# Kernel tuning notes

Hardware: AMD Instinct MI355X
Metric: run time of the kernel (lower is better)

## Reference

```python
import jax, jax.numpy as jnp
import numpy as np

NUM_BIRDS = 512
NUM_COLORS = 512
HIDDEN = 128
NUM_LAYERS = 3


def setup_inputs() -> dict:
    key = jax.random.key(0)
    ks = jax.random.split(key, 12)
    s = 0.05
    H = HIDDEN
    L = NUM_LAYERS
    inp = {
        "probs": jax.random.uniform(ks[0], (NUM_BIRDS, NUM_COLORS), dtype=jnp.float32),
        "node_proj_w": jax.random.normal(ks[1], (NUM_COLORS, H), dtype=jnp.float32) * s,
        "node_proj_b": jnp.zeros((H,), dtype=jnp.float32),
        "edge_w1": jax.random.normal(ks[2], (L, 2 * H, H), dtype=jnp.float32) * s,
        "edge_b1": jnp.zeros((L, H), dtype=jnp.float32),
        "edge_w2": jax.random.normal(ks[3], (L, H, H), dtype=jnp.float32) * s,
        "edge_b2": jnp.zeros((L, H), dtype=jnp.float32),
        "node_w1": jax.random.normal(ks[4], (L, 2 * H, H), dtype=jnp.float32) * s,
        "node_b1": jnp.zeros((L, H), dtype=jnp.float32),
        "node_w2": jax.random.normal(ks[5], (L, H, H), dtype=jnp.float32) * s,
        "node_b2": jnp.zeros((L, H), dtype=jnp.float32),
        "color_proj_w": jax.random.normal(ks[6], (H, NUM_COLORS), dtype=jnp.float32) * s,
        "color_proj_b": jnp.zeros((NUM_COLORS,), dtype=jnp.float32),
    }
    return inp


def reference(probs, node_proj_w, node_proj_b, edge_w1, edge_b1, edge_w2, edge_b2,
              node_w1, node_b1, node_w2, node_b2, color_proj_w, color_proj_b):
    B, C = probs.shape  # num_birds, num_colors
    H = node_proj_w.shape[1]
    N = B + C  # total bipartite nodes

    # top-k filtering (k = num_birds); scatter values back into a zero matrix
    vals, idx = jax.lax.top_k(probs, B)  # (B, B)
    rows = jnp.arange(B)[:, None]
    filtered = jnp.zeros_like(probs).at[rows, idx].set(vals)

    # bipartite node features: projected filtered probs + projected one-hot colors
    bird_nodes = filtered @ node_proj_w + node_proj_b          # (B, H)
    color_nodes = node_proj_w + node_proj_b                    # eye(C) @ W + b -> (C, H)
    x = jnp.concatenate([bird_nodes, color_nodes], axis=0)     # (N, H)

    # fully-connected bipartite edge list
    row = jnp.repeat(jnp.arange(B), C)          # (E,)
    col = jnp.tile(jnp.arange(C), B) + B        # (E,)

    for l in range(edge_w1.shape[0]):
        # edge model: gather endpoints, 2-layer MLP per edge
        ef = jnp.concatenate([x[row], x[col]], axis=1)                     # (E, 2H)
        e = jnp.maximum(ef @ edge_w1[l] + edge_b1[l], 0.0) @ edge_w2[l] + edge_b2[l]
        # node model: scatter-add edge features to both endpoints
        aggr = jnp.zeros((N, H), dtype=x.dtype).at[row].add(e).at[col].add(e)
        nf = jnp.concatenate([x, aggr], axis=1)                            # (N, 2H)
        x = jnp.maximum(nf @ node_w1[l] + node_b1[l], 0.0) @ node_w2[l] + node_b2[l]
        # dropout is eval-mode identity

    gnn_scores = x[:B] @ color_proj_w + color_proj_b  # (B, C)

    # combined score only where color j is in bird i's top-k set
    mask = jnp.zeros((B, C), dtype=probs.dtype).at[rows, idx].set(1.0)
    combined = gnn_scores * probs * mask

    # Hungarian cost matrix: cost[i, j] = 1 - combined[i, top_k_indices[i, j]]
    cost = 1.0 - jnp.take_along_axis(combined, idx, axis=1)  # (B, B)
    return cost
```

## Files before the change

### kernel.cpp

```cpp
#include <hip/hip_runtime.h>

#define NB 512
#define NC 512
#define HD 128
typedef float2 f2;
typedef float4 f4;

#define ACC8(SRC, WP, KQ) { const f2* W2_ = (const f2*)(WP); \
  _Pragma("unroll 8") for (int kk_ = 0; kk_ < (KQ); ++kk_) { \
    int k_ = slot * (KQ) + kk_; \
    f2 w_ = W2_[k_ * 64 + cg]; \
    float s0_ = SRC[0][k_], s1_ = SRC[1][k_], s2_ = SRC[2][k_], s3_ = SRC[3][k_]; \
    a0 = fmaf(s0_, w_.x, a0); a1 = fmaf(s0_, w_.y, a1); \
    a2 = fmaf(s1_, w_.x, a2); a3 = fmaf(s1_, w_.y, a3); \
    a4 = fmaf(s2_, w_.x, a4); a5 = fmaf(s2_, w_.y, a5); \
    a6 = fmaf(s3_, w_.x, a6); a7 = fmaf(s3_, w_.y, a7); } }
#define ZACC() { a0=a1=a2=a3=a4=a5=a6=a7=0.f; }
#define WRPART() { *(f2*)&part[slot][0][c0] = make_float2(a0, a1); \
  *(f2*)&part[slot][1][c0] = make_float2(a2, a3); \
  *(f2*)&part[slot][2][c0] = make_float2(a4, a5); \
  *(f2*)&part[slot][3][c0] = make_float2(a6, a7); }
#define PSUM(r_, cc_) (part[0][r_][cc_] + part[1][r_][cc_] + part[2][r_][cc_] + \
                       part[3][r_][cc_] + part[4][r_][cc_] + part[5][r_][cc_] + \
                       part[6][r_][cc_] + part[7][r_][cc_])

__global__ __launch_bounds__(512) void k_pre(
    const float* __restrict__ probs, const float* __restrict__ npw,
    const float* __restrict__ npb, const float* __restrict__ ew1,
    const float* __restrict__ eb1, float* __restrict__ x0,
    float* __restrict__ u, float* __restrict__ v, int* __restrict__ idx) {
  __shared__ float srt[2][NC];
  __shared__ float As[4][NC];
  __shared__ float xs[4][HD];
  __shared__ float part[8][4][HD];
  const int tid = threadIdx.x, b = blockIdx.x;
  const int cg = tid & 63, slot = tid >> 6;
  const int c0 = 2 * cg;
  float a0, a1, a2, a3, a4, a5, a6, a7;

  {
    const int h = tid >> 8, e = tid & 255;
    const int srow = 2 * b + h;
    srt[h][e]       = probs[srow * NC + e];
    srt[h][e + 256] = probs[srow * NC + e + 256];
    __syncthreads();
    const float v0 = srt[h][e], v1 = srt[h][e + 256];
    int r0_ = 0, r1_ = 0;
#pragma unroll 8
    for (int j4 = 0; j4 < 128; ++j4) {
      f4 sv = ((const f4*)&srt[h][0])[j4];
      int j = 4 * j4;
      r0_ += (sv.x > v0) || (sv.x == v0 && (j + 0) < e);
      r0_ += (sv.y > v0) || (sv.y == v0 && (j + 1) < e);
      r0_ += (sv.z > v0) || (sv.z == v0 && (j + 2) < e);
      r0_ += (sv.w > v0) || (sv.w == v0 && (j + 3) < e);
      r1_ += (sv.x > v1) || (sv.x == v1 && (j + 0) < e + 256);
      r1_ += (sv.y > v1) || (sv.y == v1 && (j + 1) < e + 256);
      r1_ += (sv.z > v1) || (sv.z == v1 && (j + 2) < e + 256);
      r1_ += (sv.w > v1) || (sv.w == v1 && (j + 3) < e + 256);
    }
    idx[srow * NC + r0_] = e;
    idx[srow * NC + r1_] = e + 256;
  }

  if (b < 128) {
    const int r0 = b * 4;
    ((f4*)As)[tid] = ((const f4*)(probs + r0 * NC))[tid];
    __syncthreads();
    ZACC(); ACC8(As, npw, 64);
    WRPART();
    __syncthreads();
    { int r = tid >> 7, cc = tid & 127;
      float val = PSUM(r, cc) + npb[cc];
      xs[r][cc] = val;
      x0[(r0 + r) * HD + cc] = val; }
    __syncthreads();
    ZACC(); ACC8(xs, ew1, 16);
    WRPART();
    __syncthreads();
    { int r = tid >> 7, cc = tid & 127;
      u[(r0 + r) * HD + cc] = PSUM(r, cc) + eb1[cc]; }
  } else {
    const int cr0 = (b - 128) * 4;
    { int r = tid >> 7, cc = tid & 127;
      float val = npw[(cr0 + r) * HD + cc] + npb[cc];
      xs[r][cc] = val;
      x0[(NB + cr0 + r) * HD + cc] = val; }
    __syncthreads();
    ZACC(); ACC8(xs, ew1 + HD * HD, 16);
    WRPART();
    __syncthreads();
    { int r = tid >> 7, cc = tid & 127;
      v[(cr0 + r) * HD + cc] = PSUM(r, cc); }
  }
}

__global__ __launch_bounds__(512) void k_RSlayer(
    const float* __restrict__ xin, const float* __restrict__ uin,
    const float* __restrict__ vin,
    const float* __restrict__ ew2l, const float* __restrict__ eb2l,
    const float* __restrict__ nw1l, const float* __restrict__ nb1l,
    const float* __restrict__ nw2l, const float* __restrict__ nb2l,
    const float* __restrict__ ew1n, const float* __restrict__ eb1n,
    float* __restrict__ xout, float* __restrict__ uout, float* __restrict__ vout) {
  __shared__ float rsp[16][HD];
  __shared__ float xa[4][HD], rs[4][HD], ag[4][HD], h1[4][HD], xo[4][HD];
  __shared__ float part[8][4][HD];
  const int tid = threadIdx.x, b = blockIdx.x;
  const int cg = tid & 63, slot = tid >> 6;
  const int c0 = 2 * cg;
  const int nr0 = b * 4;
  const bool bird = b < 128;
  const int r0s = (b & 127) * 4;
  float a0, a1, a2, a3, a4, a5, a6, a7;

  if (tid < 256) ((f2*)xa)[tid] = ((const f2*)(xin + nr0 * HD))[tid];

  {
    const float* mine  = bird ? uin : vin;
    const float* other = bird ? vin : uin;
    const int s16 = tid >> 5, cg32 = tid & 31;
    const int row = s16 & 3, jq = s16 >> 2;
    f4 base = *(const f4*)&mine[(r0s + row) * HD + 4 * cg32];
    const f4* O4 = (const f4*)other;
    f4 acc = make_float4(0.f, 0.f, 0.f, 0.f);
#pragma unroll 8
    for (int j = jq * 128; j < jq * 128 + 128; ++j) {
      f4 o = O4[j * 32 + cg32];
      acc.x += fmaxf(base.x + o.x, 0.f);
      acc.y += fmaxf(base.y + o.y, 0.f);
      acc.z += fmaxf(base.z + o.z, 0.f);
      acc.w += fmaxf(base.w + o.w, 0.f);
    }
    *(f4*)&rsp[s16][4 * cg32] = acc;
  }
  __syncthreads();
  { int r = tid >> 7, cc = tid & 127;
    rs[r][cc] = rsp[r][cc] + rsp[4 + r][cc] + rsp[8 + r][cc] + rsp[12 + r][cc]; }
  __syncthreads();

  ZACC(); ACC8(rs, ew2l, 16);
  WRPART();
  __syncthreads();
  { int r = tid >> 7, cc = tid & 127;
    ag[r][cc] = PSUM(r, cc) + 512.f * eb2l[cc]; }
  __syncthreads();

  ZACC();
  ACC8(xa, nw1l, 16);
  ACC8(ag, nw1l + HD * HD, 16);
  WRPART();
  __syncthreads();
  { int r = tid >> 7, cc = tid & 127;
    h1[r][cc] = fmaxf(PSUM(r, cc) + nb1l[cc], 0.f); }
  __syncthreads();

  ZACC(); ACC8(h1, nw2l, 16);
  WRPART();
  __syncthreads();
  { int r = tid >> 7, cc = tid & 127;
    float val = PSUM(r, cc) + nb2l[cc];
    xo[r][cc] = val;
    xout[(nr0 + r) * HD + cc] = val; }
  __syncthreads();

  ZACC(); ACC8(xo, (bird ? ew1n : ew1n + HD * HD), 16);
  WRPART();
  __syncthreads();
  { int r = tid >> 7, cc = tid & 127;
    float val = PSUM(r, cc) + (bird ? eb1n[cc] : 0.f);
    if (bird) uout[(nr0 + r) * HD + cc] = val;
    else      vout[(nr0 - NB + r) * HD + cc] = val; }
}

__global__ __launch_bounds__(512) void k_last(
    const float* __restrict__ xin, const float* __restrict__ uin,
    const float* __restrict__ vin,
    const float* __restrict__ ew2l, const float* __restrict__ eb2l,
    const float* __restrict__ nw1l, const float* __restrict__ nb1l,
    const float* __restrict__ nw2l, const float* __restrict__ nb2l,
    const float* __restrict__ cpw, const float* __restrict__ cpb,
    const float* __restrict__ probs, const int* __restrict__ idx,
    float* __restrict__ out) {
  __shared__ float rsp[16][HD];
  __shared__ float xa[4][HD], rs[4][HD], ag[4][HD], h1[4][HD], xo[4][HD];
  __shared__ float part[8][4][HD];
  __shared__ float comb[4][NC];
  const int tid = threadIdx.x, b = blockIdx.x;
  const int cg = tid & 63, slot = tid >> 6;
  const int c0 = 2 * cg;
  const int nr0 = b * 4;
  float a0, a1, a2, a3, a4, a5, a6, a7;

  if (tid < 256) ((f2*)xa)[tid] = ((const f2*)(xin + nr0 * HD))[tid];

  {
    const int s16 = tid >> 5, cg32 = tid & 31;
    const int row = s16 & 3, jq = s16 >> 2;
    f4 base = *(const f4*)&uin[(nr0 + row) * HD + 4 * cg32];
    const f4* O4 = (const f4*)vin;
    f4 acc = make_float4(0.f, 0.f, 0.f, 0.f);
#pragma unroll 8
    for (int j = jq * 128; j < jq * 128 + 128; ++j) {
      f4 o = O4[j * 32 + cg32];
      acc.x += fmaxf(base.x + o.x, 0.f);
      acc.y += fmaxf(base.y + o.y, 0.f);
      acc.z += fmaxf(base.z + o.z, 0.f);
      acc.w += fmaxf(base.w + o.w, 0.f);
    }
    *(f4*)&rsp[s16][4 * cg32] = acc;
  }
  __syncthreads();
  { int r = tid >> 7, cc = tid & 127;
    rs[r][cc] = rsp[r][cc] + rsp[4 + r][cc] + rsp[8 + r][cc] + rsp[12 + r][cc]; }
  __syncthreads();

  ZACC(); ACC8(rs, ew2l, 16);
  WRPART();
  __syncthreads();
  { int r = tid >> 7, cc = tid & 127;
    ag[r][cc] = PSUM(r, cc) + 512.f * eb2l[cc]; }
  __syncthreads();

  ZACC();
  ACC8(xa, nw1l, 16);
  ACC8(ag, nw1l + HD * HD, 16);
  WRPART();
  __syncthreads();
  { int r = tid >> 7, cc = tid & 127;
    h1[r][cc] = fmaxf(PSUM(r, cc) + nb1l[cc], 0.f); }
  __syncthreads();

  ZACC(); ACC8(h1, nw2l, 16);
  WRPART();
  __syncthreads();
  { int r = tid >> 7, cc = tid & 127;
    xo[r][cc] = PSUM(r, cc) + nb2l[cc]; }
  __syncthreads();

  {
    const int c = tid;
    float s0 = cpb[c], s1 = s0, s2 = s0, s3 = s0;
#pragma unroll 8
    for (int k = 0; k < HD; ++k) {
      float w = cpw[k * NC + c];
      s0 = fmaf(xo[0][k], w, s0);
      s1 = fmaf(xo[1][k], w, s1);
      s2 = fmaf(xo[2][k], w, s2);
      s3 = fmaf(xo[3][k], w, s3);
    }
    comb[0][c] = s0 * probs[(nr0 + 0) * NC + c];
    comb[1][c] = s1 * probs[(nr0 + 1) * NC + c];
    comb[2][c] = s2 * probs[(nr0 + 2) * NC + c];
    comb[3][c] = s3 * probs[(nr0 + 3) * NC + c];
  }
  __syncthreads();
#pragma unroll
  for (int i = 0; i < 4; ++i) {
    int ii = i * 512 + tid;
    int r = ii >> 9, j = ii & 511;
    int cc = idx[(nr0 + r) * NC + j];
    out[(nr0 + r) * NC + j] = 1.f - comb[r][cc];
  }
}

extern "C" void kernel_launch(void* const* d_in, const int* in_sizes, int n_in,
                              void* d_out, int out_size, void* d_ws, size_t ws_size,
                              hipStream_t stream) {
  const float* probs = (const float*)d_in[0];
  const float* npw   = (const float*)d_in[1];
  const float* npb   = (const float*)d_in[2];
  const float* ew1   = (const float*)d_in[3];
  const float* eb1   = (const float*)d_in[4];
  const float* ew2   = (const float*)d_in[5];
  const float* eb2   = (const float*)d_in[6];
  const float* nw1   = (const float*)d_in[7];
  const float* nb1   = (const float*)d_in[8];
  const float* nw2   = (const float*)d_in[9];
  const float* nb2   = (const float*)d_in[10];
  const float* cpw   = (const float*)d_in[11];
  const float* cpb   = (const float*)d_in[12];
  float* out = (float*)d_out;

  float* x0 = (float*)d_ws;
  float* x1 = x0 + 1024 * HD;
  float* ua = x1 + 1024 * HD;
  float* va = ua + NB * HD;
  float* ub = va + NC * HD;
  float* vb = ub + NB * HD;
  int*  idx = (int*)(vb + NC * HD);

  k_pre    <<<256, 512, 0, stream>>>(probs, npw, npb, ew1, eb1, x0, ua, va, idx);
  k_RSlayer<<<256, 512, 0, stream>>>(x0, ua, va, ew2, eb2, nw1, nb1, nw2, nb2,
                                     ew1 + 32768, eb1 + HD, x1, ub, vb);
  k_RSlayer<<<256, 512, 0, stream>>>(x1, ub, vb, ew2 + 16384, eb2 + HD,
                                     nw1 + 32768, nb1 + HD, nw2 + 16384, nb2 + HD,
                                     ew1 + 65536, eb1 + 2 * HD, x0, ua, va);
  k_last   <<<128, 512, 0, stream>>>(x0, ua, va, ew2 + 32768, eb2 + 2 * HD,
                                     nw1 + 65536, nb1 + 2 * HD,
                                     nw2 + 32768, nb2 + 2 * HD,
                                     cpw, cpb, probs, idx, out);
}
```

Before: 89.62 us.

## Fuse all layer kernels into one persistent kernel with grid barriers

Replaces four sequential kernel launches with a single persistent kernel of 256 blocks that synchronise through an atomic grid barrier in workspace memory. Each block keeps its node features and edge-projection rows in shared memory across layers, so x no longer round-trips through global memory. Launch gaps and the global reloads of x should go away. In exchange it adds a memset per call, spin-wait barrier latency, and a reliance on all 256 blocks being resident at once.

After: 266.6 us. +197.5%, slower.

```diff
diff --git a/kernel.cpp b/kernel.cpp
--- a/kernel.cpp
+++ b/kernel.cpp
@@ -6,49 +6,127 @@
 typedef float2 f2;
 typedef float4 f4;
 
-#define ACC8(SRC, WP, KQ) { const f2* W2_ = (const f2*)(WP); \
+#define ACC8S(SB, SSTR, WP, KQ) { const f2* W2_ = (const f2*)(WP); const float* S_ = (SB); \
   _Pragma("unroll 8") for (int kk_ = 0; kk_ < (KQ); ++kk_) { \
     int k_ = slot * (KQ) + kk_; \
     f2 w_ = W2_[k_ * 64 + cg]; \
-    float s0_ = SRC[0][k_], s1_ = SRC[1][k_], s2_ = SRC[2][k_], s3_ = SRC[3][k_]; \
+    float s0_ = S_[k_], s1_ = S_[(SSTR) + k_], s2_ = S_[2*(SSTR) + k_], s3_ = S_[3*(SSTR) + k_]; \
     a0 = fmaf(s0_, w_.x, a0); a1 = fmaf(s0_, w_.y, a1); \
     a2 = fmaf(s1_, w_.x, a2); a3 = fmaf(s1_, w_.y, a3); \
     a4 = fmaf(s2_, w_.x, a4); a5 = fmaf(s2_, w_.y, a5); \
     a6 = fmaf(s3_, w_.x, a6); a7 = fmaf(s3_, w_.y, a7); } }
 #define ZACC() { a0=a1=a2=a3=a4=a5=a6=a7=0.f; }
-#define WRPART() { *(f2*)&part[slot][0][c0] = make_float2(a0, a1); \
-  *(f2*)&part[slot][1][c0] = make_float2(a2, a3); \
-  *(f2*)&part[slot][2][c0] = make_float2(a4, a5); \
-  *(f2*)&part[slot][3][c0] = make_float2(a6, a7); }
-#define PSUM(r_, cc_) (part[0][r_][cc_] + part[1][r_][cc_] + part[2][r_][cc_] + \
-                       part[3][r_][cc_] + part[4][r_][cc_] + part[5][r_][cc_] + \
-                       part[6][r_][cc_] + part[7][r_][cc_])
-
-__global__ __launch_bounds__(512) void k_pre(
+#define WRPART() { float* P_ = part + slot * 512; \
+  *(f2*)&P_[c0]     = make_float2(a0, a1); *(f2*)&P_[128 + c0] = make_float2(a2, a3); \
+  *(f2*)&P_[256 + c0] = make_float2(a4, a5); *(f2*)&P_[384 + c0] = make_float2(a6, a7); }
+#define PSUM(r_, cc_) (part[(r_)*128+(cc_)] + part[512+(r_)*128+(cc_)] + \
+  part[1024+(r_)*128+(cc_)] + part[1536+(r_)*128+(cc_)] + part[2048+(r_)*128+(cc_)] + \
+  part[2560+(r_)*128+(cc_)] + part[3072+(r_)*128+(cc_)] + part[3584+(r_)*128+(cc_)])
+
+__device__ __forceinline__ void gbar(unsigned* bar, unsigned target) {
+  __syncthreads();
+  if (threadIdx.x == 0) {
+    __threadfence();
+    __hip_atomic_fetch_add(bar, 1u, __ATOMIC_RELEASE, __HIP_MEMORY_SCOPE_AGENT);
+    while (__hip_atomic_load(bar, __ATOMIC_ACQUIRE, __HIP_MEMORY_SCOPE_AGENT) < target)
+      __builtin_amdgcn_s_sleep(2);
+  }
+  __syncthreads();
+  __threadfence();
+}
+
+__device__ __forceinline__ void phaseT(
+    int tid, int cg, int slot, int c0, bool bird, int rside,
+    float* xa, float* um, float* part, float* rsp, float* rs, float* ag,
+    float* h1, float* xo, const float* other,
+    const float* ew2l, const float* eb2l, const float* nw1l, const float* nb1l,
+    const float* nw2l, const float* nb2l, const float* ew1n, const float* eb1n,
+    float* mine_out) {
+  float a0, a1, a2, a3, a4, a5, a6, a7;
+  {
+    const int s16 = tid >> 5, cg32 = tid & 31;
+    const int row = s16 & 3, jq = s16 >> 2;
+    f4 base = *(const f4*)&um[row * HD + 4 * cg32];
+    const f4* O4 = (const f4*)other;
+    f4 acc = make_float4(0.f, 0.f, 0.f, 0.f);
+#pragma unroll 8
+    for (int j = jq * 128; j < jq * 128 + 128; ++j) {
+      f4 o = O4[j * 32 + cg32];
+      acc.x += fmaxf(base.x + o.x, 0.f);
+      acc.y += fmaxf(base.y + o.y, 0.f);
+      acc.z += fmaxf(base.z + o.z, 0.f);
+      acc.w += fmaxf(base.w + o.w, 0.f);
+    }
+    *(f4*)&rsp[s16 * HD + 4 * cg32] = acc;
+  }
+  __syncthreads();
+  { int r = tid >> 7, cc = tid & 127;
+    rs[r * HD + cc] = rsp[r * HD + cc] + rsp[(4 + r) * HD + cc] +
+                      rsp[(8 + r) * HD + cc] + rsp[(12 + r) * HD + cc]; }
+  __syncthreads();
+  ZACC(); ACC8S(rs, HD, ew2l, 16); WRPART();
+  __syncthreads();
+  { int r = tid >> 7, cc = tid & 127;
+    ag[r * HD + cc] = PSUM(r, cc) + 512.f * eb2l[cc]; }
+  __syncthreads();
+  ZACC(); ACC8S(xa, HD, nw1l, 16); ACC8S(ag, HD, nw1l + HD * HD, 16);
+  WRPART();
+  __syncthreads();
+  { int r = tid >> 7, cc = tid & 127;
+    h1[r * HD + cc] = fmaxf(PSUM(r, cc) + nb1l[cc], 0.f); }
+  __syncthreads();
+  ZACC(); ACC8S(h1, HD, nw2l, 16); WRPART();
+  __syncthreads();
+  { int r = tid >> 7, cc = tid & 127;
+    xo[r * HD + cc] = PSUM(r, cc) + nb2l[cc]; }
+  __syncthreads();
+  ZACC(); ACC8S(xo, HD, bird ? ew1n : ew1n + HD * HD, 16); WRPART();
+  __syncthreads();
+  { int r = tid >> 7, cc = tid & 127;
+    float uval = PSUM(r, cc) + (bird ? eb1n[cc] : 0.f);
+    um[r * HD + cc] = uval;
+    if (mine_out) mine_out[(rside + r) * HD + cc] = uval;
+    xa[r * HD + cc] = xo[r * HD + cc]; }
+}
+
+__global__ __launch_bounds__(512) void mega(
     const float* __restrict__ probs, const float* __restrict__ npw,
     const float* __restrict__ npb, const float* __restrict__ ew1,
-    const float* __restrict__ eb1, float* __restrict__ x0,
-    float* __restrict__ u, float* __restrict__ v, int* __restrict__ idx) {
-  __shared__ float srt[2][NC];
-  __shared__ float As[4][NC];
-  __shared__ float xs[4][HD];
-  __shared__ float part[8][4][HD];
+    const float* __restrict__ eb1, const float* __restrict__ ew2,
+    const float* __restrict__ eb2, const float* __restrict__ nw1,
+    const float* __restrict__ nb1, const float* __restrict__ nw2,
+    const float* __restrict__ nb2, const float* __restrict__ cpw,
+    const float* __restrict__ cpb, float* __restrict__ out,
+    float* ug0, float* ug1, float* vg0, float* vg1,
+    int* idx, unsigned* bar) {
+  __shared__ float xa[4 * HD];
+  __shared__ float um[4 * HD];
+  __shared__ float scr[10240];
+  float* part = scr;
+  float* rsp  = scr + 4096;
+  float* rs   = scr + 6144;
+  float* ag   = scr + 6656;
+  float* h1   = scr + 7168;
+  float* xo   = scr + 7680;
   const int tid = threadIdx.x, b = blockIdx.x;
   const int cg = tid & 63, slot = tid >> 6;
   const int c0 = 2 * cg;
+  const bool bird = b < 128;
+  const int rside = (b & 127) * 4;
   float a0, a1, a2, a3, a4, a5, a6, a7;
 
   {
+    float* srt = scr + 4096;
     const int h = tid >> 8, e = tid & 255;
     const int srow = 2 * b + h;
-    srt[h][e]       = probs[srow * NC + e];
-    srt[h][e + 256] = probs[srow * NC + e + 256];
-    __syncthreads();
-    const float v0 = srt[h][e], v1 = srt[h][e + 256];
+    srt[h * 512 + e]       = probs[srow * NC + e];
+    srt[h * 512 + e + 256] = probs[srow * NC + e + 256];
+    __syncthreads();
+    const float v0 = srt[h * 512 + e], v1 = srt[h * 512 + e + 256];
     int r0_ = 0, r1_ = 0;
 #pragma unroll 8
     for (int j4 = 0; j4 < 128; ++j4) {
-      f4 sv = ((const f4*)&srt[h][0])[j4];
+      f4 sv = ((const f4*)(srt + h * 512))[j4];
       int j = 4 * j4;
       r0_ += (sv.x > v0) || (sv.x == v0 && (j + 0) < e);
       r0_ += (sv.y > v0) || (sv.y == v0 && (j + 1) < e);
@@ -61,206 +139,113 @@
     }
     idx[srow * NC + r0_] = e;
     idx[srow * NC + r1_] = e + 256;
-  }
-
-  if (b < 128) {
-    const int r0 = b * 4;
-    ((f4*)As)[tid] = ((const f4*)(probs + r0 * NC))[tid];
-    __syncthreads();
-    ZACC(); ACC8(As, npw, 64);
+    __syncthreads();
+  }
+
+  if (bird) {
+    float* As = scr + 5120;
+    ((f4*)As)[tid] = ((const f4*)(probs + rside * NC))[tid];
+    __syncthreads();
+    ZACC(); ACC8S(As, 512, npw, 64); WRPART();
+    __syncthreads();
+    { int r = tid >> 7, cc = tid & 127;
+      xa[r * HD + cc] = PSUM(r, cc) + npb[cc]; }
+    __syncthreads();
+    ZACC(); ACC8S(xa, HD, ew1, 16); WRPART();
+    __syncthreads();
+    { int r = tid >> 7, cc = tid & 127;
+      float uval = PSUM(r, cc) + eb1[cc];
+      um[r * HD + cc] = uval;
+      ug0[(rside + r) * HD + cc] = uval; }
+  } else {
+    { int r = tid >> 7, cc = tid & 127;
+      xa[r * HD + cc] = npw[(rside + r) * HD + cc] + npb[cc]; }
+    __syncthreads();
+    ZACC(); ACC8S(xa, HD, ew1 + HD * HD, 16); WRPART();
+    __syncthreads();
+    { int r = tid >> 7, cc = tid & 127;
+      float vval = PSUM(r, cc);
+      um[r * HD + cc] = vval;
+      vg0[(rside + r) * HD + cc] = vval; }
+  }
+  gbar(bar, 256);
+
+  phaseT(tid, cg, slot, c0, bird, rside, xa, um, part, rsp, rs, ag, h1, xo,
+         bird ? vg0 : ug0, ew2, eb2, nw1, nb1, nw2, nb2,
+         ew1 + 32768, eb1 + HD, bird ? ug1 : vg1);
+  gbar(bar, 512);
+  phaseT(tid, cg, slot, c0, bird, rside, xa, um, part, rsp, rs, ag, h1, xo,
+         bird ? vg1 : ug1, ew2 + 16384, eb2 + HD, nw1 + 32768, nb1 + HD,
+         nw2 + 16384, nb2 + HD, ew1 + 65536, eb1 + 2 * HD,
+         bird ? (float*)nullptr : vg0);
+  gbar(bar, 768);
+  if (!bird) return;
+
+  {
+    const float* ew2l = ew2 + 32768; const float* eb2l = eb2 + 256;
+    const float* nw1l = nw1 + 65536; const float* nb1l = nb1 + 256;
+    const float* nw2l = nw2 + 32768; const float* nb2l = nb2 + 256;
+    {
+      const int s16 = tid >> 5, cg32 = tid & 31;
+      const int row = s16 & 3, jq = s16 >> 2;
+      f4 base = *(const f4*)&um[row * HD + 4 * cg32];
+      const f4* O4 = (const f4*)vg0;
+      f4 acc = make_float4(0.f, 0.f, 0.f, 0.f);
+#pragma unroll 8
+      for (int j = jq * 128; j < jq * 128 + 128; ++j) {
+        f4 o = O4[j * 32 + cg32];
+        acc.x += fmaxf(base.x + o.x, 0.f);
+        acc.y += fmaxf(base.y + o.y, 0.f);
+        acc.z += fmaxf(base.z + o.z, 0.f);
+        acc.w += fmaxf(base.w + o.w, 0.f);
+      }
+      *(f4*)&rsp[s16 * HD + 4 * cg32] = acc;
+    }
+    __syncthreads();
+    { int r = tid >> 7, cc = tid & 127;
+      rs[r * HD + cc] = rsp[r * HD + cc] + rsp[(4 + r) * HD + cc] +
+                        rsp[(8 + r) * HD + cc] + rsp[(12 + r) * HD + cc]; }
+    __syncthreads();
+    ZACC(); ACC8S(rs, HD, ew2l, 16); WRPART();
+    __syncthreads();
+    { int r = tid >> 7, cc = tid & 127;
+      ag[r * HD + cc] = PSUM(r, cc) + 512.f * eb2l[cc]; }
+    __syncthreads();
+    ZACC(); ACC8S(xa, HD, nw1l, 16); ACC8S(ag, HD, nw1l + HD * HD, 16);
     WRPART();
     __syncthreads();
     { int r = tid >> 7, cc = tid & 127;
-      float val = PSUM(r, cc) + npb[cc];
-      xs[r][cc] = val;
-      x0[(r0 + r) * HD + cc] = val; }
-    __syncthreads();
-    ZACC(); ACC8(xs, ew1, 16);
-    WRPART();
-    __syncthreads();
-    { int r = tid >> 7, cc = tid & 127;
-      u[(r0 + r) * HD + cc] = PSUM(r, cc) + eb1[cc]; }
-  } else {
-    const int cr0 = (b - 128) * 4;
-    { int r = tid >> 7, cc = tid & 127;
-      float val = npw[(cr0 + r) * HD + cc] + npb[cc];
-      xs[r][cc] = val;
-      x0[(NB + cr0 + r) * HD + cc] = val; }
-    __syncthreads();
-    ZACC(); ACC8(xs, ew1 + HD * HD, 16);
-    WRPART();
-    __syncthreads();
-    { int r = tid >> 7, cc = tid & 127;
-      v[(cr0 + r) * HD + cc] = PSUM(r, cc); }
-  }
-}
-
-__global__ __launch_bounds__(512) void k_RSlayer(
-    const float* __restrict__ xin, const float* __restrict__ uin,
-    const float* __restrict__ vin,
-    const float* __restrict__ ew2l, const float* __restrict__ eb2l,
-    const float* __restrict__ nw1l, const float* __restrict__ nb1l,
-    const float* __restrict__ nw2l, const float* __restrict__ nb2l,
-    const float* __restrict__ ew1n, const float* __restrict__ eb1n,
-    float* __restrict__ xout, float* __restrict__ uout, float* __restrict__ vout) {
-  __shared__ float rsp[16][HD];
-  __shared__ float xa[4][HD], rs[4][HD], ag[4][HD], h1[4][HD], xo[4][HD];
-  __shared__ float part[8][4][HD];
-  const int tid = threadIdx.x, b = blockIdx.x;
-  const int cg = tid & 63, slot = tid >> 6;
-  const int c0 = 2 * cg;
-  const int nr0 = b * 4;
-  const bool bird = b < 128;
-  const int r0s = (b & 127) * 4;
-  float a0, a1, a2, a3, a4, a5, a6, a7;
-
-  if (tid < 256) ((f2*)xa)[tid] = ((const f2*)(xin + nr0 * HD))[tid];
-
-  {
-    const float* mine  = bird ? uin : vin;
-    const float* other = bird ? vin : uin;
-    const int s16 = tid >> 5, cg32 = tid & 31;
-    const int row = s16 & 3, jq = s16 >> 2;
-    f4 base = *(const f4*)&mine[(r0s + row) * HD + 4 * cg32];
-    const f4* O4 = (const f4*)other;
-    f4 acc = make_float4(0.f, 0.f, 0.f, 0.f);
-#pragma unroll 8
-    for (int j = jq * 128; j < jq * 128 + 128; ++j) {
-      f4 o = O4[j * 32 + cg32];
-      acc.x += fmaxf(base.x + o.x, 0.f);
-      acc.y += fmaxf(base.y + o.y, 0.f);
-      acc.z += fmaxf(base.z + o.z, 0.f);
-      acc.w += fmaxf(base.w + o.w, 0.f);
-    }
-    *(f4*)&rsp[s16][4 * cg32] = acc;
-  }
-  __syncthreads();
-  { int r = tid >> 7, cc = tid & 127;
-    rs[r][cc] = rsp[r][cc] + rsp[4 + r][cc] + rsp[8 + r][cc] + rsp[12 + r][cc]; }
-  __syncthreads();
-
-  ZACC(); ACC8(rs, ew2l, 16);
-  WRPART();
-  __syncthreads();
-  { int r = tid >> 7, cc = tid & 127;
-    ag[r][cc] = PSUM(r, cc) + 512.f * eb2l[cc]; }
-  __syncthreads();
-
-  ZACC();
-  ACC8(xa, nw1l, 16);
-  ACC8(ag, nw1l + HD * HD, 16);
-  WRPART();
-  __syncthreads();
-  { int r = tid >> 7, cc = tid & 127;
-    h1[r][cc] = fmaxf(PSUM(r, cc) + nb1l[cc], 0.f); }
-  __syncthreads();
-
-  ZACC(); ACC8(h1, nw2l, 16);
-  WRPART();
-  __syncthreads();
-  { int r = tid >> 7, cc = tid & 127;
-    float val = PSUM(r, cc) + nb2l[cc];
-    xo[r][cc] = val;
-    xout[(nr0 + r) * HD + cc] = val; }
-  __syncthreads();
-
-  ZACC(); ACC8(xo, (bird ? ew1n : ew1n + HD * HD), 16);
-  WRPART();
-  __syncthreads();
-  { int r = tid >> 7, cc = tid & 127;
-    float val = PSUM(r, cc) + (bird ? eb1n[cc] : 0.f);
-    if (bird) uout[(nr0 + r) * HD + cc] = val;
-    else      vout[(nr0 - NB + r) * HD + cc] = val; }
-}
-
-__global__ __launch_bounds__(512) void k_last(
-    const float* __restrict__ xin, const float* __restrict__ uin,
-    const float* __restrict__ vin,
-    const float* __restrict__ ew2l, const float* __restrict__ eb2l,
-    const float* __restrict__ nw1l, const float* __restrict__ nb1l,
-    const float* __restrict__ nw2l, const float* __restrict__ nb2l,
-    const float* __restrict__ cpw, const float* __restrict__ cpb,
-    const float* __restrict__ probs, const int* __restrict__ idx,
-    float* __restrict__ out) {
-  __shared__ float rsp[16][HD];
-  __shared__ float xa[4][HD], rs[4][HD], ag[4][HD], h1[4][HD], xo[4][HD];
-  __shared__ float part[8][4][HD];
-  __shared__ float comb[4][NC];
-  const int tid = threadIdx.x, b = blockIdx.x;
-  const int cg = tid & 63, slot = tid >> 6;
-  const int c0 = 2 * cg;
-  const int nr0 = b * 4;
-  float a0, a1, a2, a3, a4, a5, a6, a7;
-
-  if (tid < 256) ((f2*)xa)[tid] = ((const f2*)(xin + nr0 * HD))[tid];
-
-  {
-    const int s16 = tid >> 5, cg32 = tid & 31;
-    const int row = s16 & 3, jq = s16 >> 2;
-    f4 base = *(const f4*)&uin[(nr0 + row) * HD + 4 * cg32];
-    const f4* O4 = (const f4*)vin;
-    f4 acc = make_float4(0.f, 0.f, 0.f, 0.f);
-#pragma unroll 8
-    for (int j = jq * 128; j < jq * 128 + 128; ++j) {
-      f4 o = O4[j * 32 + cg32];
-      acc.x += fmaxf(base.x + o.x, 0.f);
-      acc.y += fmaxf(base.y + o.y, 0.f);
-      acc.z += fmaxf(base.z + o.z, 0.f);
-      acc.w += fmaxf(base.w + o.w, 0.f);
-    }
-    *(f4*)&rsp[s16][4 * cg32] = acc;
-  }
-  __syncthreads();
-  { int r = tid >> 7, cc = tid & 127;
-    rs[r][cc] = rsp[r][cc] + rsp[4 + r][cc] + rsp[8 + r][cc] + rsp[12 + r][cc]; }
-  __syncthreads();
-
-  ZACC(); ACC8(rs, ew2l, 16);
-  WRPART();
-  __syncthreads();
-  { int r = tid >> 7, cc = tid & 127;
-    ag[r][cc] = PSUM(r, cc) + 512.f * eb2l[cc]; }
-  __syncthreads();
-
-  ZACC();
-  ACC8(xa, nw1l, 16);
-  ACC8(ag, nw1l + HD * HD, 16);
-  WRPART();
-  __syncthreads();
-  { int r = tid >> 7, cc = tid & 127;
-    h1[r][cc] = fmaxf(PSUM(r, cc) + nb1l[cc], 0.f); }
-  __syncthreads();
-
-  ZACC(); ACC8(h1, nw2l, 16);
-  WRPART();
-  __syncthreads();
-  { int r = tid >> 7, cc = tid & 127;
-    xo[r][cc] = PSUM(r, cc) + nb2l[cc]; }
-  __syncthreads();
-
-  {
-    const int c = tid;
-    float s0 = cpb[c], s1 = s0, s2 = s0, s3 = s0;
-#pragma unroll 8
-    for (int k = 0; k < HD; ++k) {
-      float w = cpw[k * NC + c];
-      s0 = fmaf(xo[0][k], w, s0);
-      s1 = fmaf(xo[1][k], w, s1);
-      s2 = fmaf(xo[2][k], w, s2);
-      s3 = fmaf(xo[3][k], w, s3);
-    }
-    comb[0][c] = s0 * probs[(nr0 + 0) * NC + c];
-    comb[1][c] = s1 * probs[(nr0 + 1) * NC + c];
-    comb[2][c] = s2 * probs[(nr0 + 2) * NC + c];
-    comb[3][c] = s3 * probs[(nr0 + 3) * NC + c];
-  }
-  __syncthreads();
+      h1[r * HD + cc] = fmaxf(PSUM(r, cc) + nb1l[cc], 0.f); }
+    __syncthreads();
+    ZACC(); ACC8S(h1, HD, nw2l, 16); WRPART();
+    __syncthreads();
+    { int r = tid >> 7, cc = tid & 127;
+      xo[r * HD + cc] = PSUM(r, cc) + nb2l[cc]; }
+    __syncthreads();
+    float* comb = scr + 4096;
+    {
+      float s0 = cpb[tid], s1 = s0, s2 = s0, s3 = s0;
+#pragma unroll 8
+      for (int k = 0; k < HD; ++k) {
+        float w = cpw[k * NC + tid];
+        s0 = fmaf(xo[k], w, s0);
+        s1 = fmaf(xo[HD + k], w, s1);
+        s2 = fmaf(xo[2 * HD + k], w, s2);
+        s3 = fmaf(xo[3 * HD + k], w, s3);
+      }
+      comb[tid]        = s0 * probs[(rside + 0) * NC + tid];
+      comb[512 + tid]  = s1 * probs[(rside + 1) * NC + tid];
+      comb[1024 + tid] = s2 * probs[(rside + 2) * NC + tid];
+      comb[1536 + tid] = s3 * probs[(rside + 3) * NC + tid];
+    }
+    __syncthreads();
 #pragma unroll
-  for (int i = 0; i < 4; ++i) {
-    int ii = i * 512 + tid;
-    int r = ii >> 9, j = ii & 511;
-    int cc = idx[(nr0 + r) * NC + j];
-    out[(nr0 + r) * NC + j] = 1.f - comb[r][cc];
+    for (int i = 0; i < 4; ++i) {
+      int ii = i * 512 + tid;
+      int r = ii >> 9, j = ii & 511;
+      int cc = idx[(rside + r) * NC + j];
+      out[(rside + r) * NC + j] = 1.f - comb[r * 512 + cc];
+    }
   }
 }
 
@@ -280,24 +265,17 @@
   const float* nb2   = (const float*)d_in[10];
   const float* cpw   = (const float*)d_in[11];
   const float* cpb   = (const float*)d_in[12];
-  float* out = (float*)d_out;
-
-  float* x0 = (float*)d_ws;
-  float* x1 = x0 + 1024 * HD;
-  float* ua = x1 + 1024 * HD;
-  float* va = ua + NB * HD;
-  float* ub = va + NC * HD;
-  float* vb = ub + NB * HD;
-  int*  idx = (int*)(vb + NC * HD);
-
-  k_pre    <<<256, 512, 0, stream>>>(probs, npw, npb, ew1, eb1, x0, ua, va, idx);
-  k_RSlayer<<<256, 512, 0, stream>>>(x0, ua, va, ew2, eb2, nw1, nb1, nw2, nb2,
-                                     ew1 + 32768, eb1 + HD, x1, ub, vb);
-  k_RSlayer<<<256, 512, 0, stream>>>(x1, ub, vb, ew2 + 16384, eb2 + HD,
-                                     nw1 + 32768, nb1 + HD, nw2 + 16384, nb2 + HD,
-                                     ew1 + 65536, eb1 + 2 * HD, x0, ua, va);
-  k_last   <<<128, 512, 0, stream>>>(x0, ua, va, ew2 + 32768, eb2 + 2 * HD,
-                                     nw1 + 65536, nb1 + 2 * HD,
-                                     nw2 + 32768, nb2 + 2 * HD,
-                                     cpw, cpb, probs, idx, out);
-}
+
+  unsigned* bar = (unsigned*)d_ws;
+  float* base = (float*)d_ws + 1024;
+  float* ug0 = base;
+  float* ug1 = ug0 + NB * HD;
+  float* vg0 = ug1 + NB * HD;
+  float* vg1 = vg0 + NC * HD;
+  int*  idx  = (int*)(vg1 + NC * HD);
+
+  hipMemsetAsync(d_ws, 0, 4096, stream);
+  mega<<<256, 512, 0, stream>>>(probs, npw, npb, ew1, eb1, ew2, eb2,
+                                nw1, nb1, nw2, nb2, cpw, cpb,
+                                (float*)d_out, ug0, ug1, vg0, vg1, idx, bar);
+}
```

## Move top-k rank sort out of k_pre into extra blocks of first layer

Applied to the files above, without the earlier changes.

The per-row rank-based top-k index computation moves out of k_pre and into 128 extra blocks appended to the first k_RSlayer launch (grid 384). There each block ranks 4 rows with one element per thread, reusing the rsp shared buffer. The aim is to shorten the critical path of k_pre and let the sort run concurrently with the layer-1 work. Several loop unroll factors also rise from 8 to 16, at the cost of more register pressure.

Measured after the change: 117.6 us. +31.2%, slower.

```diff
diff --git a/kernel.cpp b/kernel.cpp
--- a/kernel.cpp
+++ b/kernel.cpp
@@ -7,7 +7,7 @@
 typedef float4 f4;
 
 #define ACC8(SRC, WP, KQ) { const f2* W2_ = (const f2*)(WP); \
-  _Pragma("unroll 8") for (int kk_ = 0; kk_ < (KQ); ++kk_) { \
+  _Pragma("unroll 16") for (int kk_ = 0; kk_ < (KQ); ++kk_) { \
     int k_ = slot * (KQ) + kk_; \
     f2 w_ = W2_[k_ * 64 + cg]; \
     float s0_ = SRC[0][k_], s1_ = SRC[1][k_], s2_ = SRC[2][k_], s3_ = SRC[3][k_]; \
@@ -28,8 +28,7 @@
     const float* __restrict__ probs, const float* __restrict__ npw,
     const float* __restrict__ npb, const float* __restrict__ ew1,
     const float* __restrict__ eb1, float* __restrict__ x0,
-    float* __restrict__ u, float* __restrict__ v, int* __restrict__ idx) {
-  __shared__ float srt[2][NC];
+    float* __restrict__ u, float* __restrict__ v) {
   __shared__ float As[4][NC];
   __shared__ float xs[4][HD];
   __shared__ float part[8][4][HD];
@@ -37,31 +36,6 @@
   const int cg = tid & 63, slot = tid >> 6;
   const int c0 = 2 * cg;
   float a0, a1, a2, a3, a4, a5, a6, a7;
-
-  {
-    const int h = tid >> 8, e = tid & 255;
-    const int srow = 2 * b + h;
-    srt[h][e]       = probs[srow * NC + e];
-    srt[h][e + 256] = probs[srow * NC + e + 256];
-    __syncthreads();
-    const float v0 = srt[h][e], v1 = srt[h][e + 256];
-    int r0_ = 0, r1_ = 0;
-#pragma unroll 8
-    for (int j4 = 0; j4 < 128; ++j4) {
-      f4 sv = ((const f4*)&srt[h][0])[j4];
-      int j = 4 * j4;
-      r0_ += (sv.x > v0) || (sv.x == v0 && (j + 0) < e);
-      r0_ += (sv.y > v0) || (sv.y == v0 && (j + 1) < e);
-      r0_ += (sv.z > v0) || (sv.z == v0 && (j + 2) < e);
-      r0_ += (sv.w > v0) || (sv.w == v0 && (j + 3) < e);
-      r1_ += (sv.x > v1) || (sv.x == v1 && (j + 0) < e + 256);
-      r1_ += (sv.y > v1) || (sv.y == v1 && (j + 1) < e + 256);
-      r1_ += (sv.z > v1) || (sv.z == v1 && (j + 2) < e + 256);
-      r1_ += (sv.w > v1) || (sv.w == v1 && (j + 3) < e + 256);
-    }
-    idx[srow * NC + r0_] = e;
-    idx[srow * NC + r1_] = e + 256;
-  }
 
   if (b < 128) {
     const int r0 = b * 4;
@@ -102,11 +76,37 @@
     const float* __restrict__ nw1l, const float* __restrict__ nb1l,
     const float* __restrict__ nw2l, const float* __restrict__ nb2l,
     const float* __restrict__ ew1n, const float* __restrict__ eb1n,
-    float* __restrict__ xout, float* __restrict__ uout, float* __restrict__ vout) {
+    float* __restrict__ xout, float* __restrict__ uout, float* __restrict__ vout,
+    const float* __restrict__ probs, int* __restrict__ idx) {
   __shared__ float rsp[16][HD];
   __shared__ float xa[4][HD], rs[4][HD], ag[4][HD], h1[4][HD], xo[4][HD];
   __shared__ float part[8][4][HD];
   const int tid = threadIdx.x, b = blockIdx.x;
+
+  if (b >= 256) {
+    float* srt = &rsp[0][0];
+    const int r0 = (b - 256) * 4;
+    for (int i = tid; i < 4 * NC; i += 512) srt[i] = probs[r0 * NC + i];
+    __syncthreads();
+#pragma unroll
+    for (int r = 0; r < 4; ++r) {
+      const float* row = srt + r * NC;
+      const float myv = row[tid];
+      int rank = 0;
+#pragma unroll 16
+      for (int j4 = 0; j4 < 128; ++j4) {
+        f4 sv = ((const f4*)row)[j4];
+        int j = 4 * j4;
+        rank += (sv.x > myv) || (sv.x == myv && (j + 0) < tid);
+        rank += (sv.y > myv) || (sv.y == myv && (j + 1) < tid);
+        rank += (sv.z > myv) || (sv.z == myv && (j + 2) < tid);
+        rank += (sv.w > myv) || (sv.w == myv && (j + 3) < tid);
+      }
+      idx[(r0 + r) * NC + rank] = tid;
+    }
+    return;
+  }
+
   const int cg = tid & 63, slot = tid >> 6;
   const int c0 = 2 * cg;
   const int nr0 = b * 4;
@@ -124,7 +124,7 @@
     f4 base = *(const f4*)&mine[(r0s + row) * HD + 4 * cg32];
     const f4* O4 = (const f4*)other;
     f4 acc = make_float4(0.f, 0.f, 0.f, 0.f);
-#pragma unroll 8
+#pragma unroll 16
     for (int j = jq * 128; j < jq * 128 + 128; ++j) {
       f4 o = O4[j * 32 + cg32];
       acc.x += fmaxf(base.x + o.x, 0.f);
@@ -200,7 +200,7 @@
     f4 base = *(const f4*)&uin[(nr0 + row) * HD + 4 * cg32];
     const f4* O4 = (const f4*)vin;
     f4 acc = make_float4(0.f, 0.f, 0.f, 0.f);
-#pragma unroll 8
+#pragma unroll 16
     for (int j = jq * 128; j < jq * 128 + 128; ++j) {
       f4 o = O4[j * 32 + cg32];
       acc.x += fmaxf(base.x + o.x, 0.f);
@@ -241,7 +241,7 @@
   {
     const int c = tid;
     float s0 = cpb[c], s1 = s0, s2 = s0, s3 = s0;
-#pragma unroll 8
+#pragma unroll 16
     for (int k = 0; k < HD; ++k) {
       float w = cpw[k * NC + c];
       s0 = fmaf(xo[0][k], w, s0);
@@ -290,12 +290,14 @@
   float* vb = ub + NB * HD;
   int*  idx = (int*)(vb + NC * HD);
 
-  k_pre    <<<256, 512, 0, stream>>>(probs, npw, npb, ew1, eb1, x0, ua, va, idx);
-  k_RSlayer<<<256, 512, 0, stream>>>(x0, ua, va, ew2, eb2, nw1, nb1, nw2, nb2,
-                                     ew1 + 32768, eb1 + HD, x1, ub, vb);
+  k_pre    <<<256, 512, 0, stream>>>(probs, npw, npb, ew1, eb1, x0, ua, va);
+  k_RSlayer<<<384, 512, 0, stream>>>(x0, ua, va, ew2, eb2, nw1, nb1, nw2, nb2,
+                                     ew1 + 32768, eb1 + HD, x1, ub, vb,
+                                     probs, idx);
   k_RSlayer<<<256, 512, 0, stream>>>(x1, ub, vb, ew2 + 16384, eb2 + HD,
                                      nw1 + 32768, nb1 + HD, nw2 + 16384, nb2 + HD,
-                                     ew1 + 65536, eb1 + 2 * HD, x0, ua, va);
+                                     ew1 + 65536, eb1 + 2 * HD, x0, ua, va,
+                                     probs, idx);
   k_last   <<<128, 512, 0, stream>>>(x0, ua, va, ew2 + 32768, eb2 + 2 * HD,
                                      nw1 + 65536, nb1 + 2 * HD,
                                      nw2 + 32768, nb2 + 2 * HD,
```
